# Performance work log

Hardware: AMD Instinct MI355X
Metric: run time of the kernel (lower is better)

The kernel has to match this reference:

```python
import jax, jax.numpy as jnp
import numpy as np

T, B, E, H = 64, 64, 128, 256
N_ITEMS, N_DATA = 50000, 20000
EPS = 1e-8


def setup_inputs() -> dict:
    key = jax.random.key(0)
    ks = jax.random.split(key, 20)
    lengths = jnp.sort(jax.random.randint(ks[0], (B,), 1, T + 1))[::-1]
    lengths = lengths.at[0].set(T)  # pack_padded_sequence expects max length first
    x = jax.random.randint(ks[1], (T, B), 1, N_ITEMS)
    tmask = jnp.arange(T)[:, None] < lengths[None, :]
    x = jnp.where(tmask, x, 0)  # padding index 0
    s = 0.05
    emb_table = (jax.random.normal(ks[2], (N_ITEMS, E)) * s).at[0].set(0.0)  # padding_idx=0
    data_embeddings = jax.random.normal(ks[3], (N_DATA, E)) * s
    return {
        'x': x, 'lengths': lengths,
        'emb_table': emb_table, 'data_embeddings': data_embeddings,
        'W_ih': jax.random.normal(ks[4], (4 * H, E)) * s,
        'W_hh': jax.random.normal(ks[5], (4 * H, H)) * s,
        'b_ih': jax.random.normal(ks[6], (4 * H,)) * s,
        'b_hh': jax.random.normal(ks[7], (4 * H,)) * s,
        'Wq': jax.random.normal(ks[8], (H, H)) * s, 'bq': jax.random.normal(ks[9], (H,)) * s,
        'Wk': jax.random.normal(ks[10], (H, H)) * s, 'bk': jax.random.normal(ks[11], (H,)) * s,
        'Wv': jax.random.normal(ks[12], (H, H)) * s, 'bv': jax.random.normal(ks[13], (H,)) * s,
        'W_out': jax.random.normal(ks[14], (E, H)) * s, 'b_out': jax.random.normal(ks[15], (E,)) * s,
    }


def _forward(x, lengths, emb_table, data_embeddings, W_ih, W_hh, b_ih, b_hh,
             Wq, bq, Wk, bk, Wv, bv, W_out, b_out):
    t_len, b_sz = x.shape
    e_dim = emb_table.shape[1]
    h_dim = W_hh.shape[1]

    embs0 = emb_table[x]  # (T, B, E); dropout is identity in eval mode
    initial_embs = jax.lax.stop_gradient(embs0)  # .clone().detach() in original

    # PositionalEncoding: original slices by x.size(1) == batch dim (faithful quirk)
    pos = jnp.arange(b_sz, dtype=jnp.float32)[:, None]
    div = jnp.exp(jnp.arange(0, e_dim, 2, dtype=jnp.float32) * (-jnp.log(10000.0) / e_dim))
    enc = jnp.stack([jnp.sin(pos * div), jnp.cos(pos * div)], axis=-1).reshape(b_sz, e_dim)
    embs = embs0 + enc[None, :, :]  # broadcast over time

    # single-layer LSTM over time (gate order i, f, g, o)
    def step(carry, x_t):
        h, c = carry
        gates = x_t @ W_ih.T + h @ W_hh.T + (b_ih + b_hh)  # (B, 4H)
        i, f, g, o = jnp.split(gates, 4, axis=-1)
        c = jax.nn.sigmoid(f) * c + jax.nn.sigmoid(i) * jnp.tanh(g)
        h = jax.nn.sigmoid(o) * jnp.tanh(c)
        return (h, c), h

    h0 = jnp.zeros((b_sz, h_dim), embs.dtype)
    (_, _), lstm_out = jax.lax.scan(step, (h0, h0), embs)  # (T, B, H)

    # pack/pad round-trip zeroes outputs past each length (LSTM is causal)
    tmask = jnp.arange(t_len)[:, None] < lengths[None, :]  # (T, B)
    lstm_out = lstm_out * tmask[:, :, None]
    lstm_out = lstm_out.transpose(1, 0, 2)  # (B, T, H)

    padding_mask = jnp.sum(lstm_out, axis=-1) != 0  # (B, T)

    q = lstm_out @ Wq.T + bq
    k = lstm_out @ Wk.T + bk
    v = lstm_out @ Wv.T + bv
    score = jnp.einsum('bth,bsh->bts', q, k) / jnp.sqrt(jnp.float32(h_dim))
    score = jnp.where(padding_mask[:, None, :], score, -jnp.inf)
    attn = jax.nn.softmax(score, axis=2)
    weighted = jnp.einsum('bts,bsh->bth', attn, v)  # (B, T, H)
    attn_output = jnp.mean(weighted, axis=1) @ W_out.T + b_out  # (B, E)

    # kNN: fused normalize + matmul + argmin + gather over all T at once
    qn = initial_embs / jnp.clip(jnp.linalg.norm(initial_embs, axis=-1, keepdims=True), EPS)
    dn = data_embeddings / jnp.clip(jnp.linalg.norm(data_embeddings, axis=-1, keepdims=True), EPS)
    sims = jnp.einsum('tbe,ne->tbn', qn, dn)  # (T, B, N_DATA)
    idx = jnp.argmax(sims, axis=-1)  # argmin of (1 - sim)
    closest = jnp.mean(data_embeddings[idx], axis=0)  # (B, E)

    attn_output = attn_output * closest
    return attn_output @ emb_table.T  # (B, n_items)


def reference(x, lengths, emb_table, data_embeddings, W_ih, W_hh, b_ih, b_hh,
              Wq, bq, Wk, bk, Wv, bv, W_out, b_out):
    return _forward(x, lengths, emb_table, data_embeddings, W_ih, W_hh, b_ih, b_hh,
                    Wq, bq, Wk, bk, Wv, bv, W_out, b_out)
```

## Files before the change

### kernel.cpp

```cpp
#include <hip/hip_runtime.h>

typedef unsigned int uint;
typedef unsigned short ushort;
typedef unsigned long long u64;

#define NITEMS 50000
#define NDATA  20000
#define BLKCAP 4096u
#define OVCAP  65536u

#define OFF_LSTMOUT   0x0000000ULL
#define OFF_HX        0x0400000ULL
#define OFF_HXM       0x0440000ULL
#define OFF_PACKED    0x0480000ULL
#define OFF_PACKED2   0x0488000ULL
#define OFF_HITCNTS   0x0490000ULL
#define OFF_OHITCNT   0x0490800ULL
#define MEMSET_BYTES  0x0491000ULL
#define OFF_QMARGIN   0x0491000ULL
#define OFF_XW        0x05A0000ULL
#define OFF_QKV       0x15A0000ULL
#define OFF_HITBUF    OFF_QKV
#define OFF_WIHT      0x21A0000ULL
#define OFF_WQKVT     0x2220000ULL
#define OFF_BIASIH    0x22E0000ULL
#define OFF_BQKV      0x22E1000ULL
#define OFF_DNSCALE   0x22E2000ULL
#define OFF_CLOSEST   0x22F6000ULL
#define OFF_AV        0x22FE000ULL
#define OFF_DEMB16    0x2306000ULL
#define OFF_A16       0x27E8000ULL
#define OFF_OVF       0x28E8000ULL

__device__ __forceinline__ ushort f2bf(float f) {
  union { float f; uint u; } v; v.f = f;
  uint u = v.u;
  return (ushort)((u + 0x7FFFu + ((u >> 16) & 1u)) >> 16);
}
__device__ __forceinline__ uint fkey(float f) {
  union { float f; uint u; } v; v.f = f;
  return (v.u & 0x80000000u) ? ~v.u : (v.u | 0x80000000u);
}
__device__ __forceinline__ u64 shfl_xor_u64(u64 v, int off) {
  uint lo = (uint)v, hi = (uint)(v >> 32);
  lo = (uint)__shfl_xor((int)lo, off);
  hi = (uint)__shfl_xor((int)hi, off);
  return ((u64)hi << 32) | (u64)lo;
}

typedef __attribute__((ext_vector_type(8))) short short8;
typedef __attribute__((ext_vector_type(4))) float floatx4;

#define R32(M) M(0) M(1) M(2) M(3) M(4) M(5) M(6) M(7) M(8) M(9) M(10) M(11) \
  M(12) M(13) M(14) M(15) M(16) M(17) M(18) M(19) M(20) M(21) M(22) M(23) \
  M(24) M(25) M(26) M(27) M(28) M(29) M(30) M(31)

#define HIX(j) ((j) + (((j) >> 7) << 2))

#define LBAR() do { \
  __builtin_amdgcn_sched_barrier(0); \
  asm volatile("s_waitcnt lgkmcnt(0)" ::: "memory"); \
  __builtin_amdgcn_s_barrier(); \
  __builtin_amdgcn_sched_barrier(0); \
} while (0)

__global__ __launch_bounds__(256) void prep_kernel(
    const int* __restrict__ x,
    const float* __restrict__ emb, const float* __restrict__ demb,
    const float* __restrict__ W_ih,
    const float* __restrict__ Wq, const float* __restrict__ Wk, const float* __restrict__ Wv,
    const float* __restrict__ b_ih, const float* __restrict__ b_hh,
    const float* __restrict__ bq, const float* __restrict__ bk, const float* __restrict__ bv,
    float* __restrict__ dnscale, ushort* __restrict__ demb16, ushort* __restrict__ a16,
    float* __restrict__ wiht, float* __restrict__ wqkvt,
    float* __restrict__ biasih, float* __restrict__ bqkv,
    float* __restrict__ qmargin, u64* __restrict__ packed2)
{
  int blk = blockIdx.x, tid = threadIdx.x;
  if (blk < 5000) {
    int row = blk * 4 + (tid >> 6);
    int lane = tid & 63;
    float2 d = *(const float2*)(demb + (size_t)row * 128 + lane * 2);
    float s = d.x * d.x + d.y * d.y;
    for (int off = 32; off; off >>= 1) s += __shfl_xor(s, off);
    if (lane == 0) dnscale[row] = 1.0f / fmaxf(sqrtf(s), 1e-8f);
  } else if (blk < 6250) {
    size_t base = ((size_t)(blk - 5000) * 256 + tid) * 8;
    float4 f1 = *(const float4*)(demb + base);
    float4 f2 = *(const float4*)(demb + base + 4);
    uint4 o;
    o.x = (uint)f2bf(f1.x) | ((uint)f2bf(f1.y) << 16);
    o.y = (uint)f2bf(f1.z) | ((uint)f2bf(f1.w) << 16);
    o.z = (uint)f2bf(f2.x) | ((uint)f2bf(f2.y) << 16);
    o.w = (uint)f2bf(f2.z) | ((uint)f2bf(f2.w) << 16);
    *(uint4*)(demb16 + base) = o;
  } else if (blk < 6506) {
    int idx = (blk - 6250) * 256 + tid;
    int m = idx >> 4, seg = idx & 15;
    const float* src = emb + (size_t)x[m] * 128 + seg * 8;
    float4 f1 = *(const float4*)(src);
    float4 f2 = *(const float4*)(src + 4);
    uint4 o;
    o.x = (uint)f2bf(f1.x) | ((uint)f2bf(f1.y) << 16);
    o.y = (uint)f2bf(f1.z) | ((uint)f2bf(f1.w) << 16);
    o.z = (uint)f2bf(f2.x) | ((uint)f2bf(f2.y) << 16);
    o.w = (uint)f2bf(f2.z) | ((uint)f2bf(f2.w) << 16);
    *(uint4*)(a16 + (size_t)m * 128 + seg * 8) = o;
  } else if (blk < 7018) {
    int f = (blk - 6506) * 256 + tid;
    int r = f >> 7, e = f & 127;
    wiht[e * 1024 + r] = W_ih[f];
  } else if (blk < 7786) {
    int f = (blk - 7018) * 256 + tid;
    int w = f >> 16; int rem = f & 65535;
    int r = rem >> 8, e = rem & 255;
    const float* src = (w == 0) ? Wq : (w == 1) ? Wk : Wv;
    wqkvt[e * 768 + w * 256 + r] = src[rem];
  } else if (blk < 7790) {
    int idx = (blk - 7786) * 256 + tid;
    if (idx < 1024) biasih[idx] = b_ih[idx] + b_hh[idx];
  } else if (blk < 7793) {
    int idx = (blk - 7790) * 256 + tid;
    if (idx < 768) {
      int w = idx >> 8; int r = idx & 255;
      const float* src = (w == 0) ? bq : (w == 1) ? bk : bv;
      bqkv[idx] = src[r];
    }
  } else {
    int row = (blk - 7793) * 4 + (tid >> 6);
    int lane = tid & 63;
    float2 d = *(const float2*)(emb + (size_t)x[row] * 128 + lane * 2);
    float s = d.x * d.x + d.y * d.y;
    for (int off = 32; off; off >>= 1) s += __shfl_xor(s, off);
    if (lane == 0) {
      if (s == 0.f) {
        qmargin[row] = -1e30f;
        packed2[row] = ((u64)fkey(0.0f) << 32) | 0xFFFFFFFFull;
      } else {
        qmargin[row] = 0.017f * sqrtf(s) + 1e-5f;
      }
    }
  }
}

__global__ __launch_bounds__(256) void xw_kernel(
    const int* __restrict__ x, const float* __restrict__ emb,
    const float* __restrict__ wiht, const float* __restrict__ biasih,
    float* __restrict__ xW)
{
  __shared__ __align__(16) float At[128 * 16];
  int blk = blockIdx.x, tid = threadIdx.x;
  int m0 = blk * 16;
  for (int c = 0; c < 8; ++c) {
    int idx = c * 256 + tid;
    int mm = idx >> 7, e = idx & 127;
    int m = m0 + mm;
    int bcol = m & 63;
    int xv = x[m];
    float val = emb[(size_t)xv * 128 + e];
    int j = e >> 1;
    float arg = (float)bcol * __expf((float)j * -0.14391157f);
    val += (e & 1) ? cosf(arg) : sinf(arg);
    At[e * 16 + mm] = val;
  }
  __syncthreads();
  int quad = tid >> 6, l = tid & 63;
  for (int rp = 0; rp < 4; ++rp) {
    int r = rp * 256 + l * 4;
    float acc[4][4] = {};
    for (int e = 0; e < 128; ++e) {
      float4 wv4 = *(const float4*)(wiht + e * 1024 + r);
      float4 av4 = *(const float4*)(At + e * 16 + quad * 4);
      float am[4] = {av4.x, av4.y, av4.z, av4.w};
      float wr4[4] = {wv4.x, wv4.y, wv4.z, wv4.w};
      #pragma unroll
      for (int mi = 0; mi < 4; ++mi)
        #pragma unroll
        for (int ri = 0; ri < 4; ++ri)
          acc[mi][ri] += am[mi] * wr4[ri];
    }
    float4 bv4 = *(const float4*)(biasih + r);
    #pragma unroll
    for (int mi = 0; mi < 4; ++mi) {
      size_t m = (size_t)(m0 + quad * 4 + mi);
      float4 o;
      o.x = acc[mi][0] + bv4.x; o.y = acc[mi][1] + bv4.y;
      o.z = acc[mi][2] + bv4.z; o.w = acc[mi][3] + bv4.w;
      *(float4*)(xW + m * 1024 + r) = o;
    }
  }
}

__global__ __launch_bounds__(256) void knn_kernel(
    const ushort* __restrict__ a16, const ushort* __restrict__ demb16,
    const float* __restrict__ dnscale, const float* __restrict__ qmargin,
    u64* __restrict__ packed, uint* __restrict__ hitcnts, uint* __restrict__ ohitcnt,
    uint* __restrict__ hitbuf, uint* __restrict__ ovbuf,
    const int* __restrict__ x, const float* __restrict__ emb,
    const float* __restrict__ demb, u64* __restrict__ packed2)
{
  __shared__ __align__(16) ushort b_sh[2][64 * 144];
  __shared__ uint lcnt;
  int blk = blockIdx.x, tid = threadIdx.x;
  int chunk = blk & 15, mt = blk >> 4;
  int wv = tid >> 6, lane = tid & 63;
  int col = lane & 15, quad = lane >> 4;
  int M0 = mt * 128;
  if (tid == 0) lcnt = 0;
  short8 afrag[2][4];
  #pragma unroll
  for (int s = 0; s < 2; ++s) {
    int mrow = M0 + s * 64 + wv * 16 + col;
    #pragma unroll
    for (int kf = 0; kf < 4; ++kf)
      afrag[s][kf] = *(const short8*)(a16 + (size_t)mrow * 128 + kf * 32 + quad * 8);
  }
  float best[2][4] = {{-1e30f,-1e30f,-1e30f,-1e30f},{-1e30f,-1e30f,-1e30f,-1e30f}};
  int bidx[2][4] = {};
  int nbase = chunk * 1250, nend = nbase + 1250;
  const int niter = 20;
  int srow = tid >> 4, sseg = tid & 15;
  uint4 stg[4]; float scr[4];

  #pragma unroll
  for (int p = 0; p < 4; ++p) {
    int n = nbase + p * 16 + srow;
    uint4 v = {0u,0u,0u,0u};
    if (n < nend) v = *(const uint4*)(demb16 + (size_t)n * 128 + sseg * 8);
    stg[p] = v;
  }
  #pragma unroll
  for (int ns = 0; ns < 4; ++ns) {
    int n = nbase + ns * 16 + col;
    scr[ns] = (n < nend) ? dnscale[n] : 0.f;
  }
  for (int it = 0; it < niter; ++it) {
    int n0 = nbase + it * 64;
    ushort* bsh = b_sh[it & 1];
    #pragma unroll
    for (int p = 0; p < 4; ++p)
      *(uint4*)(&bsh[(p * 16 + srow) * 144 + sseg * 8]) = stg[p];
    float mysc[4] = {scr[0], scr[1], scr[2], scr[3]};
    __syncthreads();
    if (it + 1 < niter) {
      int nb = n0 + 64;
      #pragma unroll
      for (int p = 0; p < 4; ++p) {
        int n = nb + p * 16 + srow;
        uint4 v = {0u,0u,0u,0u};
        if (n < nend) v = *(const uint4*)(demb16 + (size_t)n * 128 + sseg * 8);
        stg[p] = v;
      }
      #pragma unroll
      for (int ns = 0; ns < 4; ++ns) {
        int n = nb + ns * 16 + col;
        scr[ns] = (n < nend) ? dnscale[n] : 0.f;
      }
    }
    #pragma unroll
    for (int ns = 0; ns < 4; ++ns) {
      short8 bfr[4];
      #pragma unroll
      for (int kf = 0; kf < 4; ++kf)
        bfr[kf] = *(const short8*)(&bsh[(ns * 16 + col) * 144 + kf * 32 + quad * 8]);
      int n = n0 + ns * 16 + col;
      float sc = mysc[ns];
      bool valid = (n < nend);
      #pragma unroll
      for (int s = 0; s < 2; ++s) {
        floatx4 acc = {0.f, 0.f, 0.f, 0.f};
        #pragma unroll
        for (int kf = 0; kf < 4; ++kf)
          acc = __builtin_amdgcn_mfma_f32_16x16x32_bf16(afrag[s][kf], bfr[kf], acc, 0, 0, 0);
        #pragma unroll
        for (int r = 0; r < 4; ++r) {
          float sim = acc[r] * sc;
          if (valid && sim > best[s][r]) { best[s][r] = sim; bidx[s][r] = n; }
        }
      }
    }
  }
  float thr[2][4];
  #pragma unroll
  for (int s = 0; s < 2; ++s)
    #pragma unroll
    for (int r = 0; r < 4; ++r) {
      u64 p = ((u64)fkey(best[s][r]) << 32) | (u64)(0xFFFFFFFFu - (uint)bidx[s][r]);
      #pragma unroll
      for (int off = 1; off < 16; off <<= 1) {
        u64 o = shfl_xor_u64(p, off);
        if (o > p) p = o;
      }
      int m = M0 + s * 64 + wv * 16 + quad * 4 + r;
      union { uint u; float f; } bu;
      uint k = (uint)(p >> 32);
      bu.u = (k & 0x80000000u) ? (k & 0x7FFFFFFFu) : ~k;
      thr[s][r] = bu.f - qmargin[m];
      if (col == 0)
        atomicMax((unsigned long long*)&packed[m], (unsigned long long)p);
    }
  __syncthreads();

  uint* myregion = hitbuf + (size_t)blk * BLKCAP;
  uint* ovregion = ovbuf;
  #pragma unroll
  for (int p = 0; p < 4; ++p) {
    int n = nbase + p * 16 + srow;
    uint4 v = {0u,0u,0u,0u};
    if (n < nend) v = *(const uint4*)(demb16 + (size_t)n * 128 + sseg * 8);
    stg[p] = v;
  }
  #pragma unroll
  for (int ns = 0; ns < 4; ++ns) {
    int n = nbase + ns * 16 + col;
    scr[ns] = (n < nend) ? dnscale[n] : 0.f;
  }
  for (int it = 0; it < niter; ++it) {
    int n0 = nbase + it * 64;
    ushort* bsh = b_sh[it & 1];
    #pragma unroll
    for (int p = 0; p < 4; ++p)
      *(uint4*)(&bsh[(p * 16 + srow) * 144 + sseg * 8]) = stg[p];
    float mysc[4] = {scr[0], scr[1], scr[2], scr[3]};
    __syncthreads();
    if (it + 1 < niter) {
      int nb = n0 + 64;
      #pragma unroll
      for (int p = 0; p < 4; ++p) {
        int n = nb + p * 16 + srow;
        uint4 v = {0u,0u,0u,0u};
        if (n < nend) v = *(const uint4*)(demb16 + (size_t)n * 128 + sseg * 8);
        stg[p] = v;
      }
      #pragma unroll
      for (int ns = 0; ns < 4; ++ns) {
        int n = nb + ns * 16 + col;
        scr[ns] = (n < nend) ? dnscale[n] : 0.f;
      }
    }
    #pragma unroll
    for (int ns = 0; ns < 4; ++ns) {
      short8 bfr[4];
      #pragma unroll
      for (int kf = 0; kf < 4; ++kf)
        bfr[kf] = *(const short8*)(&bsh[(ns * 16 + col) * 144 + kf * 32 + quad * 8]);
      int n = n0 + ns * 16 + col;
      float sc = mysc[ns];
      bool valid = (n < nend);
      #pragma unroll
      for (int s = 0; s < 2; ++s) {
        floatx4 acc = {0.f, 0.f, 0.f, 0.f};
        #pragma unroll
        for (int kf = 0; kf < 4; ++kf)
          acc = __builtin_amdgcn_mfma_f32_16x16x32_bf16(afrag[s][kf], bfr[kf], acc, 0, 0, 0);
        #pragma unroll
        for (int r = 0; r < 4; ++r) {
          float sim = acc[r] * sc;
          bool hit = valid && (sim >= thr[s][r]);
          u64 mask = __ballot(hit);
          if (mask) {
            uint lcntv = (uint)__popcll(mask);
            int leader = __ffsll((unsigned long long)mask) - 1;
            uint base = 0;
            if (lane == leader) base = atomicAdd(&lcnt, lcntv);
            base = (uint)__shfl((int)base, leader);
            if (hit) {
              uint pos = base + (uint)__popcll(mask & ((1ull << lane) - 1ull));
              uint mm = (uint)(M0 + s * 64 + wv * 16 + quad * 4 + r);
              uint rec = (mm << 15) | (uint)n;
              if (pos < BLKCAP) {
                myregion[pos] = rec;
              } else {
                uint op = atomicAdd(ohitcnt, 1u);
                if (op < OVCAP) ovregion[op] = rec;
              }
            }
          }
        }
      }
    }
  }
  __syncthreads();
  if (tid == 0) hitcnts[blk] = lcnt;
  uint rcnt = lcnt; if (rcnt > BLKCAP) rcnt = BLKCAP;
  for (uint h = tid; h < rcnt; h += 256) {
    uint rec = myregion[h];
    uint m = rec >> 15, n = rec & 0x7FFFu;
    if (m >= 4096 || n >= NDATA) continue;
    const float* qr = emb + (size_t)x[m] * 128;
    const float* dr = demb + (size_t)n * 128;
    double p = 0.0;
    #pragma unroll 8
    for (int e = 0; e < 128; e += 2) {
      float2 qv = *(const float2*)(qr + e);
      float2 dv = *(const float2*)(dr + e);
      p += (double)qv.x * (double)dv.x + (double)qv.y * (double)dv.y;
    }
    float sx = (float)(p * (double)dnscale[n]);
    u64 key = ((u64)fkey(sx) << 32) | (u64)(0xFFFFFFFFu - n);
    atomicMax((unsigned long long*)&packed2[m], (unsigned long long)key);
  }
}

__global__ __launch_bounds__(512, 2) void lstm_kernel(
    const int* __restrict__ lengths, const float* __restrict__ Whh,
    const float* __restrict__ xW, float* __restrict__ lstm_out,
    u64* __restrict__ hx, u64* __restrict__ hxm)
{
  __shared__ __align__(16) float h_sh[264];
  __shared__ float part_sh[256];
  int blk = blockIdx.x, tid = threadIdx.x;
  int b = blk & 63, q = blk >> 6;
  int row_local = tid >> 1, half = tid & 1;
  int gate = row_local >> 6, jloc = row_local & 63;
  int grow = gate * 256 + q * 64 + jloc;
  const float4* wp4 = (const float4*)(Whh + (size_t)grow * 256 + half * 128);
#define WDECL(i) float4 tt##i = wp4[i]; \
  float w##i##x = tt##i.x, w##i##y = tt##i.y, w##i##z = tt##i.z, w##i##w = tt##i.w;
  R32(WDECL)
#define WPIN(i) asm volatile("" : "+v"(w##i##x), "+v"(w##i##y), "+v"(w##i##z), "+v"(w##i##w));
  R32(WPIN)
  int len = lengths[b];
  if (tid < 256) h_sh[HIX(tid)] = 0.f;
  float cval = 0.f;
  int prm = tid - 320;
  int jr = (prm < q * 64) ? prm : prm + 64;
  bool fast_ok = true;
  int j1 = q * 64 + (tid - 64);
  float xw0 = 0.f, xw1 = 0.f, xw2 = 0.f, xw3 = 0.f;
  if (tid < 64) {
    const float* xwrow = xW + ((size_t)0 * 64 + b) * 1024 + q * 64 + tid;
    xw0 = xwrow[0]; xw1 = xwrow[256]; xw2 = xwrow[512]; xw3 = xwrow[768];
  }
  __syncthreads();
  for (int t = 0; t < len; ++t) {
    float nx0 = 0.f, nx1 = 0.f, nx2 = 0.f, nx3 = 0.f;
    if (tid < 64 && t + 1 < len) {
      const float* xwrow = xW + ((size_t)(t + 1) * 64 + b) * 1024 + q * 64 + tid;
      nx0 = xwrow[0]; nx1 = xwrow[256]; nx2 = xwrow[512]; nx3 = xwrow[768];
    }
    float hprev = 0.f;
    if (tid >= 64 && tid < 128 && t > 0) hprev = h_sh[HIX(j1)];
    const float4* h4 = (const float4*)(h_sh + half * 132);
    float a[4] = {0.f, 0.f, 0.f, 0.f};
#define WACC(i) { float4 hv_ = h4[i]; \
    a[(i) & 3] += w##i##x * hv_.x + w##i##y * hv_.y + w##i##z * hv_.z + w##i##w * hv_.w; }
    R32(WACC)
    float acc = (a[0] + a[2]) + (a[1] + a[3]);
    acc += __shfl_xor(acc, 1);
    if (!half) part_sh[row_local] = acc;
    LBAR();
    if (tid < 64) {
      float gi = part_sh[tid]       + xw0;
      float gf = part_sh[64 + tid]  + xw1;
      float gg = part_sh[128 + tid] + xw2;
      float go = part_sh[192 + tid] + xw3;
      float ii = 1.f / (1.f + __expf(-gi));
      float ff = 1.f / (1.f + __expf(-gf));
      float oo = 1.f / (1.f + __expf(-go));
      float tg = 1.f - 2.f / (1.f + __expf(2.f * gg));
      cval = ff * cval + ii * tg;
      float tc = 1.f - 2.f / (1.f + __expf(2.f * cval));
      float hv = oo * tc;
      int j = q * 64 + tid;
      union { float f; uint u; } cu; cu.f = hv;
      u64 pk = ((u64)cu.u << 32) | (u64)(uint)(t + 1);
      size_t slot = ((size_t)((t + 1) & 1) * 64 + b) * 256 + j;
      __builtin_amdgcn_sched_barrier(0);
      asm volatile("s_waitcnt vmcnt(4)" ::: "memory");
      asm volatile("global_store_dwordx2 %0, %1, off"
                   :: "v"(hxm + slot), "v"(pk) : "memory");
      __hip_atomic_store(hx + slot, pk, __ATOMIC_RELAXED, __HIP_MEMORY_SCOPE_AGENT);
      h_sh[HIX(j)] = hv;
      xw0 = nx0; xw1 = nx1; xw2 = nx2; xw3 = nx3;
    } else if (tid < 128) {
      if (t > 0) lstm_out[((size_t)b * 64 + (t - 1)) * 256 + j1] = hprev;
    } else if (tid >= 320 && t + 1 < len) {
      size_t slot = ((size_t)((t + 1) & 1) * 64 + b) * 256 + jr;
      uint want = (uint)(t + 1);
      u64 v = 0;
      bool got = false;
      if (fast_ok) {
        const u64* ms = hxm + slot;
        for (int tries = 0; tries < 32; ++tries) {
          asm volatile("global_load_dwordx2 %0, %1, off sc0\n\t"
                       "s_waitcnt vmcnt(0)"
                       : "=&v"(v) : "v"(ms) : "memory");
          if ((uint)v == want) { got = true; break; }
        }
        if (!got && t > 0) fast_ok = false;
      }
      if (!got) {
        const u64* as = hx + slot;
        int guard = 0;
        while (true) {
          v = __hip_atomic_load(as, __ATOMIC_RELAXED, __HIP_MEMORY_SCOPE_AGENT);
          if ((uint)v == want || ++guard > (1 << 24)) break;
        }
      }
      union { uint u; float f; } cv; cv.u = (uint)(v >> 32);
      h_sh[HIX(jr)] = cv.f;
    }
    LBAR();
  }
  if (tid >= 64 && tid < 128) {
    float hl = h_sh[HIX(j1)];
    lstm_out[((size_t)b * 64 + (len - 1)) * 256 + j1] = hl;
  }
}

__global__ __launch_bounds__(256) void fused_post_kernel(
    const float* __restrict__ lstm_out, const float* __restrict__ wqkvt,
    const float* __restrict__ bqkv, float* __restrict__ qkv,
    const u64* __restrict__ packed, const uint* __restrict__ ohitcnt,
    const uint* __restrict__ ovbuf, const int* __restrict__ x,
    const float* __restrict__ emb, const float* __restrict__ demb,
    const float* __restrict__ dnscale, u64* __restrict__ packed2)
{
  __shared__ __align__(16) float At[256 * 16];
  int blk = blockIdx.x, tid = threadIdx.x;
  if (blk < 256) {
    int m0 = blk * 16;
    for (int c = 0; c < 16; ++c)
      At[tid * 16 + c] = lstm_out[((size_t)m0 + c) * 256 + tid];
    __syncthreads();
    int quad = tid >> 6, l = tid & 63;
    for (int rp = 0; rp < 3; ++rp) {
      int r = rp * 256 + l * 4;
      float acc[4][4] = {};
      for (int e = 0; e < 256; ++e) {
        float4 wv4 = *(const float4*)(wqkvt + (size_t)e * 768 + r);
        float4 av4 = *(const float4*)(At + e * 16 + quad * 4);
        float am[4] = {av4.x, av4.y, av4.z, av4.w};
        float wr4[4] = {wv4.x, wv4.y, wv4.z, wv4.w};
        #pragma unroll
        for (int mi = 0; mi < 4; ++mi)
          #pragma unroll
          for (int ri = 0; ri < 4; ++ri)
            acc[mi][ri] += am[mi] * wr4[ri];
      }
      float4 bv4 = *(const float4*)(bqkv + r);
      #pragma unroll
      for (int mi = 0; mi < 4; ++mi) {
        size_t m = (size_t)(m0 + quad * 4 + mi);
        float4 o;
        o.x = acc[mi][0] + bv4.x; o.y = acc[mi][1] + bv4.y;
        o.z = acc[mi][2] + bv4.z; o.w = acc[mi][3] + bv4.w;
        *(float4*)(qkv + m * 768 + r) = o;
      }
    }
    return;
  }
  if (blk < 272) {
    uint m = (uint)(blk - 256) * 256 + tid;
    uint n = 0xFFFFFFFFu - (uint)(packed[m] & 0xFFFFFFFFull);
    if (n < NDATA) {
      const float* qr = emb + (size_t)x[m] * 128;
      const float* dr = demb + (size_t)n * 128;
      double p = 0.0;
      #pragma unroll 8
      for (int e = 0; e < 128; e += 2) {
        float2 qv = *(const float2*)(qr + e);
        float2 dv = *(const float2*)(dr + e);
        p += (double)qv.x * (double)dv.x + (double)qv.y * (double)dv.y;
      }
      float sx = (float)(p * (double)dnscale[n]);
      u64 key = ((u64)fkey(sx) << 32) | (u64)(0xFFFFFFFFu - n);
      atomicMax((unsigned long long*)&packed2[m], (unsigned long long)key);
    }
    return;
  }
  uint cnt = *ohitcnt; if (cnt > OVCAP) cnt = OVCAP;
  for (uint h = (uint)(blk - 272) * 256 + tid; h < cnt; h += 16 * 256) {
    uint rec = ovbuf[h];
    uint m = rec >> 15, n = rec & 0x7FFFu;
    if (m >= 4096 || n >= NDATA) continue;
    const float* qr = emb + (size_t)x[m] * 128;
    const float* dr = demb + (size_t)n * 128;
    double p = 0.0;
    #pragma unroll 8
    for (int e = 0; e < 128; e += 2) {
      float2 qv = *(const float2*)(qr + e);
      float2 dv = *(const float2*)(dr + e);
      p += (double)qv.x * (double)dv.x + (double)qv.y * (double)dv.y;
    }
    float sx = (float)(p * (double)dnscale[n]);
    u64 key = ((u64)fkey(sx) << 32) | (u64)(0xFFFFFFFFu - n);
    atomicMax((unsigned long long*)&packed2[m], (unsigned long long)key);
  }
}

__global__ __launch_bounds__(128) void closest_kernel(
    const u64* __restrict__ packed2, const float* __restrict__ demb,
    float* __restrict__ closest)
{
  int b = blockIdx.x, tid = threadIdx.x;
  float s = 0.f;
  for (int t = 0; t < 64; ++t) {
    uint low = (uint)(packed2[t * 64 + b] & 0xFFFFFFFFull);
    uint n = 0xFFFFFFFFu - low;
    if (n >= NDATA) n = 0;
    s += demb[(size_t)n * 128 + tid];
  }
  closest[b * 128 + tid] = s * (1.0f / 64.0f);
}

__global__ __launch_bounds__(256) void attn_kernel(
    const float* __restrict__ qkv, const int* __restrict__ lengths,
    const float* __restrict__ closest, const float* __restrict__ W_out,
    const float* __restrict__ b_out, float* __restrict__ av)
{
  __shared__ float k_sh[64 * 257];
  __shared__ __align__(16) float q_sh[4 * 256];
  __shared__ float wpart[4 * 64];
  __shared__ float wtot[64];
  __shared__ float out_sh[256];
  int b = blockIdx.x, tid = threadIdx.x;
  int wv = tid >> 6, lane = tid & 63;
  int len = lengths[b];
  for (int s = 0; s < 64; ++s)
    k_sh[s * 257 + tid] = qkv[((size_t)b * 64 + s) * 768 + 256 + tid];
  wpart[tid] = 0.f;
  for (int tq = 0; tq < 16; ++tq) {
    __syncthreads();
    #pragma unroll
    for (int c = 0; c < 4; ++c)
      q_sh[c * 256 + tid] = qkv[((size_t)b * 64 + tq * 4 + c) * 768 + tid];
    __syncthreads();
    const float* krow = k_sh + lane * 257;
    const float* qrow = q_sh + wv * 256;
    float sc = 0.f;
    #pragma unroll 8
    for (int h = 0; h < 256; ++h)
      sc += qrow[h] * krow[h];
    sc *= 0.0625f;
    bool vs = (lane < len);
    float scm = vs ? sc : -1e30f;
    float mx = scm;
    for (int off = 32; off; off >>= 1) mx = fmaxf(mx, __shfl_xor(mx, off));
    float e = vs ? __expf(sc - mx) : 0.f;
    float sum = e;
    for (int off = 32; off; off >>= 1) sum += __shfl_xor(sum, off);
    wpart[wv * 64 + lane] += e / sum;
  }
  __syncthreads();
  if (tid < 64)
    wtot[tid] = (wpart[tid] + wpart[64 + tid] + wpart[128 + tid] + wpart[192 + tid]) * (1.0f / 64.0f);
  __syncthreads();
  {
    float acc = 0.f;
    for (int s = 0; s < 64; ++s)
      acc += wtot[s] * qkv[((size_t)b * 64 + s) * 768 + 512 + tid];
    out_sh[tid] = acc;
  }
  __syncthreads();
  if (tid < 128) {
    const float4* wr = (const float4*)(W_out + (size_t)tid * 256);
    float p = b_out[tid];
    #pragma unroll
    for (int c = 0; c < 64; ++c) {
      float4 u = wr[c];
      p += out_sh[c * 4 + 0] * u.x + out_sh[c * 4 + 1] * u.y
         + out_sh[c * 4 + 2] * u.z + out_sh[c * 4 + 3] * u.w;
    }
    av[tid * 64 + b] = p * closest[b * 128 + tid];
  }
}

__global__ __launch_bounds__(256) void final_kernel(
    const float* __restrict__ emb, const float* __restrict__ av,
    float* __restrict__ out)
{
  int i = blockIdx.x * 256 + threadIdx.x;
  if (i >= NITEMS) return;
  const float4* row = (const float4*)(emb + (size_t)i * 128);
  float acc[64];
  #pragma unroll
  for (int bb = 0; bb < 64; ++bb) acc[bb] = 0.f;
  for (int e4 = 0; e4 < 32; ++e4) {
    float4 u = row[e4];
    float wvv[4] = {u.x, u.y, u.z, u.w};
    const float* ab = av + e4 * 4 * 64;
    #pragma unroll
    for (int j = 0; j < 4; ++j) {
      #pragma unroll
      for (int bb = 0; bb < 64; ++bb)
        acc[bb] += wvv[j] * ab[j * 64 + bb];
    }
  }
  #pragma unroll
  for (int bb = 0; bb < 64; ++bb)
    out[(size_t)bb * NITEMS + i] = acc[bb];
}

extern "C" void kernel_launch(void* const* d_in, const int* in_sizes, int n_in,
                              void* d_out, int out_size, void* d_ws, size_t ws_size,
                              hipStream_t stream)
{
  const int*   x       = (const int*)d_in[0];
  const int*   lengths = (const int*)d_in[1];
  const float* emb     = (const float*)d_in[2];
  const float* demb    = (const float*)d_in[3];
  const float* W_ih    = (const float*)d_in[4];
  const float* W_hh    = (const float*)d_in[5];
  const float* b_ih    = (const float*)d_in[6];
  const float* b_hh    = (const float*)d_in[7];
  const float* Wq      = (const float*)d_in[8];
  const float* bq      = (const float*)d_in[9];
  const float* Wk      = (const float*)d_in[10];
  const float* bk      = (const float*)d_in[11];
  const float* Wv      = (const float*)d_in[12];
  const float* bv      = (const float*)d_in[13];
  const float* W_out   = (const float*)d_in[14];
  const float* b_out   = (const float*)d_in[15];

  char* ws = (char*)d_ws;
  float*  lstm_out = (float*)(ws + OFF_LSTMOUT);
  u64*    hx       = (u64*)(ws + OFF_HX);
  u64*    hxm      = (u64*)(ws + OFF_HXM);
  u64*    packed   = (u64*)(ws + OFF_PACKED);
  u64*    packed2  = (u64*)(ws + OFF_PACKED2);
  uint*   hitcnts  = (uint*)(ws + OFF_HITCNTS);
  uint*   ohitcnt  = (uint*)(ws + OFF_OHITCNT);
  float*  qmargin  = (float*)(ws + OFF_QMARGIN);
  uint*   hitbuf   = (uint*)(ws + OFF_HITBUF);
  uint*   ovbuf    = (uint*)(ws + OFF_OVF);
  float*  xW       = (float*)(ws + OFF_XW);
  float*  qkv      = (float*)(ws + OFF_QKV);
  float*  wiht     = (float*)(ws + OFF_WIHT);
  float*  wqkvt    = (float*)(ws + OFF_WQKVT);
  float*  biasih   = (float*)(ws + OFF_BIASIH);
  float*  bqkv     = (float*)(ws + OFF_BQKV);
  float*  dnscale  = (float*)(ws + OFF_DNSCALE);
  float*  closest  = (float*)(ws + OFF_CLOSEST);
  float*  av       = (float*)(ws + OFF_AV);
  ushort* demb16   = (ushort*)(ws + OFF_DEMB16);
  ushort* a16      = (ushort*)(ws + OFF_A16);

  hipMemsetAsync(d_ws, 0, (size_t)MEMSET_BYTES, stream);

  hipLaunchKernelGGL(prep_kernel, dim3(8817), dim3(256), 0, stream,
                     x, emb, demb, W_ih, Wq, Wk, Wv, b_ih, b_hh, bq, bk, bv,
                     dnscale, demb16, a16, wiht, wqkvt, biasih, bqkv,
                     qmargin, packed2);
  hipLaunchKernelGGL(xw_kernel, dim3(256), dim3(256), 0, stream,
                     x, emb, wiht, biasih, xW);
  hipLaunchKernelGGL(knn_kernel, dim3(512), dim3(256), 0, stream,
                     a16, demb16, dnscale, qmargin, packed, hitcnts, ohitcnt,
                     hitbuf, ovbuf, x, emb, demb, packed2);
  hipLaunchKernelGGL(lstm_kernel, dim3(256), dim3(512), 0, stream,
                     lengths, W_hh, xW, lstm_out, hx, hxm);
  hipLaunchKernelGGL(fused_post_kernel, dim3(288), dim3(256), 0, stream,
                     lstm_out, wqkvt, bqkv, qkv, packed, ohitcnt, ovbuf,
                     x, emb, demb, dnscale, packed2);
  hipLaunchKernelGGL(closest_kernel, dim3(64), dim3(128), 0, stream,
                     packed2, demb, closest);
  hipLaunchKernelGGL(attn_kernel, dim3(64), dim3(256), 0, stream,
                     qkv, lengths, closest, W_out, b_out, av);
  hipLaunchKernelGGL(final_kernel, dim3(196), dim3(256), 0, stream,
                     emb, av, (float*)d_out);
}
```

Baseline: 584.8 us.

## Single-pass kNN with running-max threshold; fold closest into attention kernel

The kNN kernel used to sweep the data chunk twice: once for the exact per-row max, then again to collect candidates above the max minus a margin. Now it does one sweep, keeping each tile's sims in registers and collecting hits against a running threshold taken from the max so far. This removes the second MFMA pass and its reload of the bf16 data, but early tiles use a looser threshold and may record more hits, with more atomics and possible overflow. The separate closest_kernel launch is also merged into attn_kernel.

```diff
diff --git a/kernel.cpp b/kernel.cpp
--- a/kernel.cpp
+++ b/kernel.cpp
@@ -26,7 +26,6 @@
 #define OFF_BIASIH    0x22E0000ULL
 #define OFF_BQKV      0x22E1000ULL
 #define OFF_DNSCALE   0x22E2000ULL
-#define OFF_CLOSEST   0x22F6000ULL
 #define OFF_AV        0x22FE000ULL
 #define OFF_DEMB16    0x2306000ULL
 #define OFF_A16       0x27E8000ULL
@@ -217,10 +216,18 @@
   }
   float best[2][4] = {{-1e30f,-1e30f,-1e30f,-1e30f},{-1e30f,-1e30f,-1e30f,-1e30f}};
   int bidx[2][4] = {};
+  float qm[2][4];
+  #pragma unroll
+  for (int s = 0; s < 2; ++s)
+    #pragma unroll
+    for (int r = 0; r < 4; ++r)
+      qm[s][r] = qmargin[M0 + s * 64 + wv * 16 + quad * 4 + r];
   int nbase = chunk * 1250, nend = nbase + 1250;
   const int niter = 20;
   int srow = tid >> 4, sseg = tid & 15;
   uint4 stg[4]; float scr[4];
+  uint* myregion = hitbuf + (size_t)blk * BLKCAP;
+  uint* ovregion = ovbuf;
 
   #pragma unroll
   for (int p = 0; p < 4; ++p) {
@@ -257,6 +264,7 @@
         scr[ns] = (n < nend) ? dnscale[n] : 0.f;
       }
     }
+    float sims[4][2][4];
     #pragma unroll
     for (int ns = 0; ns < 4; ++ns) {
       short8 bfr[4];
@@ -274,89 +282,26 @@
           acc = __builtin_amdgcn_mfma_f32_16x16x32_bf16(afrag[s][kf], bfr[kf], acc, 0, 0, 0);
         #pragma unroll
         for (int r = 0; r < 4; ++r) {
-          float sim = acc[r] * sc;
-          if (valid && sim > best[s][r]) { best[s][r] = sim; bidx[s][r] = n; }
+          float sim = valid ? acc[r] * sc : -1e30f;
+          sims[ns][s][r] = sim;
+          if (sim > best[s][r]) { best[s][r] = sim; bidx[s][r] = n; }
         }
       }
     }
-  }
-  float thr[2][4];
-  #pragma unroll
-  for (int s = 0; s < 2; ++s)
-    #pragma unroll
-    for (int r = 0; r < 4; ++r) {
-      u64 p = ((u64)fkey(best[s][r]) << 32) | (u64)(0xFFFFFFFFu - (uint)bidx[s][r]);
-      #pragma unroll
-      for (int off = 1; off < 16; off <<= 1) {
-        u64 o = shfl_xor_u64(p, off);
-        if (o > p) p = o;
-      }
-      int m = M0 + s * 64 + wv * 16 + quad * 4 + r;
-      union { uint u; float f; } bu;
-      uint k = (uint)(p >> 32);
-      bu.u = (k & 0x80000000u) ? (k & 0x7FFFFFFFu) : ~k;
-      thr[s][r] = bu.f - qmargin[m];
-      if (col == 0)
-        atomicMax((unsigned long long*)&packed[m], (unsigned long long)p);
-    }
-  __syncthreads();
-
-  uint* myregion = hitbuf + (size_t)blk * BLKCAP;
-  uint* ovregion = ovbuf;
-  #pragma unroll
-  for (int p = 0; p < 4; ++p) {
-    int n = nbase + p * 16 + srow;
-    uint4 v = {0u,0u,0u,0u};
-    if (n < nend) v = *(const uint4*)(demb16 + (size_t)n * 128 + sseg * 8);
-    stg[p] = v;
-  }
-  #pragma unroll
-  for (int ns = 0; ns < 4; ++ns) {
-    int n = nbase + ns * 16 + col;
-    scr[ns] = (n < nend) ? dnscale[n] : 0.f;
-  }
-  for (int it = 0; it < niter; ++it) {
-    int n0 = nbase + it * 64;
-    ushort* bsh = b_sh[it & 1];
-    #pragma unroll
-    for (int p = 0; p < 4; ++p)
-      *(uint4*)(&bsh[(p * 16 + srow) * 144 + sseg * 8]) = stg[p];
-    float mysc[4] = {scr[0], scr[1], scr[2], scr[3]};
-    __syncthreads();
-    if (it + 1 < niter) {
-      int nb = n0 + 64;
-      #pragma unroll
-      for (int p = 0; p < 4; ++p) {
-        int n = nb + p * 16 + srow;
-        uint4 v = {0u,0u,0u,0u};
-        if (n < nend) v = *(const uint4*)(demb16 + (size_t)n * 128 + sseg * 8);
-        stg[p] = v;
-      }
-      #pragma unroll
-      for (int ns = 0; ns < 4; ++ns) {
-        int n = nb + ns * 16 + col;
-        scr[ns] = (n < nend) ? dnscale[n] : 0.f;
-      }
-    }
-    #pragma unroll
-    for (int ns = 0; ns < 4; ++ns) {
-      short8 bfr[4];
-      #pragma unroll
-      for (int kf = 0; kf < 4; ++kf)
-        bfr[kf] = *(const short8*)(&bsh[(ns * 16 + col) * 144 + kf * 32 + quad * 8]);
-      int n = n0 + ns * 16 + col;
-      float sc = mysc[ns];
-      bool valid = (n < nend);
-      #pragma unroll
-      for (int s = 0; s < 2; ++s) {
-        floatx4 acc = {0.f, 0.f, 0.f, 0.f};
+    #pragma unroll
+    for (int s = 0; s < 2; ++s) {
+      #pragma unroll
+      for (int r = 0; r < 4; ++r) {
+        float rb = best[s][r];
+        rb = fmaxf(rb, __shfl_xor(rb, 1));
+        rb = fmaxf(rb, __shfl_xor(rb, 2));
+        rb = fmaxf(rb, __shfl_xor(rb, 4));
+        rb = fmaxf(rb, __shfl_xor(rb, 8));
+        float thr = rb - qm[s][r];
+        uint mm = (uint)(M0 + s * 64 + wv * 16 + quad * 4 + r);
         #pragma unroll
-        for (int kf = 0; kf < 4; ++kf)
-          acc = __builtin_amdgcn_mfma_f32_16x16x32_bf16(afrag[s][kf], bfr[kf], acc, 0, 0, 0);
-        #pragma unroll
-        for (int r = 0; r < 4; ++r) {
-          float sim = acc[r] * sc;
-          bool hit = valid && (sim >= thr[s][r]);
+        for (int ns = 0; ns < 4; ++ns) {
+          bool hit = (sims[ns][s][r] >= thr);
           u64 mask = __ballot(hit);
           if (mask) {
             uint lcntv = (uint)__popcll(mask);
@@ -366,8 +311,7 @@
             base = (uint)__shfl((int)base, leader);
             if (hit) {
               uint pos = base + (uint)__popcll(mask & ((1ull << lane) - 1ull));
-              uint mm = (uint)(M0 + s * 64 + wv * 16 + quad * 4 + r);
-              uint rec = (mm << 15) | (uint)n;
+              uint rec = (mm << 15) | (uint)(n0 + ns * 16 + col);
               if (pos < BLKCAP) {
                 myregion[pos] = rec;
               } else {
@@ -380,6 +324,20 @@
       }
     }
   }
+  #pragma unroll
+  for (int s = 0; s < 2; ++s)
+    #pragma unroll
+    for (int r = 0; r < 4; ++r) {
+      u64 p = ((u64)fkey(best[s][r]) << 32) | (u64)(0xFFFFFFFFu - (uint)bidx[s][r]);
+      #pragma unroll
+      for (int off = 1; off < 16; off <<= 1) {
+        u64 o = shfl_xor_u64(p, off);
+        if (o > p) p = o;
+      }
+      int m = M0 + s * 64 + wv * 16 + quad * 4 + r;
+      if (col == 0)
+        atomicMax((unsigned long long*)&packed[m], (unsigned long long)p);
+    }
   __syncthreads();
   if (tid == 0) hitcnts[blk] = lcnt;
   uint rcnt = lcnt; if (rcnt > BLKCAP) rcnt = BLKCAP;
@@ -590,25 +548,11 @@
   }
 }
 
-__global__ __launch_bounds__(128) void closest_kernel(
-    const u64* __restrict__ packed2, const float* __restrict__ demb,
-    float* __restrict__ closest)
-{
-  int b = blockIdx.x, tid = threadIdx.x;
-  float s = 0.f;
-  for (int t = 0; t < 64; ++t) {
-    uint low = (uint)(packed2[t * 64 + b] & 0xFFFFFFFFull);
-    uint n = 0xFFFFFFFFu - low;
-    if (n >= NDATA) n = 0;
-    s += demb[(size_t)n * 128 + tid];
-  }
-  closest[b * 128 + tid] = s * (1.0f / 64.0f);
-}
-
 __global__ __launch_bounds__(256) void attn_kernel(
     const float* __restrict__ qkv, const int* __restrict__ lengths,
-    const float* __restrict__ closest, const float* __restrict__ W_out,
-    const float* __restrict__ b_out, float* __restrict__ av)
+    const u64* __restrict__ packed2, const float* __restrict__ demb,
+    const float* __restrict__ W_out, const float* __restrict__ b_out,
+    float* __restrict__ av)
 {
   __shared__ float k_sh[64 * 257];
   __shared__ __align__(16) float q_sh[4 * 256];
@@ -620,6 +564,17 @@
   int len = lengths[b];
   for (int s = 0; s < 64; ++s)
     k_sh[s * 257 + tid] = qkv[((size_t)b * 64 + s) * 768 + 256 + tid];
+  float clv = 0.f;
+  if (tid < 128) {
+    float sum = 0.f;
+    for (int t = 0; t < 64; ++t) {
+      uint low = (uint)(packed2[t * 64 + b] & 0xFFFFFFFFull);
+      uint n = 0xFFFFFFFFu - low;
+      if (n >= NDATA) n = 0;
+      sum += demb[(size_t)n * 128 + tid];
+    }
+    clv = sum * (1.0f / 64.0f);
+  }
   wpart[tid] = 0.f;
   for (int tq = 0; tq < 16; ++tq) {
     __syncthreads();
@@ -663,7 +618,7 @@
       p += out_sh[c * 4 + 0] * u.x + out_sh[c * 4 + 1] * u.y
          + out_sh[c * 4 + 2] * u.z + out_sh[c * 4 + 3] * u.w;
     }
-    av[tid * 64 + b] = p * closest[b * 128 + tid];
+    av[tid * 64 + b] = p * clv;
   }
 }
 
@@ -732,7 +687,6 @@
   float*  biasih   = (float*)(ws + OFF_BIASIH);
   float*  bqkv     = (float*)(ws + OFF_BQKV);
   float*  dnscale  = (float*)(ws + OFF_DNSCALE);
-  float*  closest  = (float*)(ws + OFF_CLOSEST);
   float*  av       = (float*)(ws + OFF_AV);
   ushort* demb16   = (ushort*)(ws + OFF_DEMB16);
   ushort* a16      = (ushort*)(ws + OFF_A16);
@@ -753,10 +707,8 @@
   hipLaunchKernelGGL(fused_post_kernel, dim3(288), dim3(256), 0, stream,
                      lstm_out, wqkvt, bqkv, qkv, packed, ohitcnt, ovbuf,
                      x, emb, demb, dnscale, packed2);
-  hipLaunchKernelGGL(closest_kernel, dim3(64), dim3(128), 0, stream,
-                     packed2, demb, closest);
   hipLaunchKernelGGL(attn_kernel, dim3(64), dim3(256), 0, stream,
-                     qkv, lengths, closest, W_out, b_out, av);
+                     qkv, lengths, packed2, demb, W_out, b_out, av);
   hipLaunchKernelGGL(final_kernel, dim3(196), dim3(256), 0, stream,
                      emb, av, (float*)d_out);
 }
```

After: 614.4 us. 1.05x slower.
